# Optimization experiments

Hardware: AMD Instinct MI355X
Metric: run time of the kernel (lower is better)

## Reference

```python
import math
import jax, jax.numpy as jnp
import numpy as np

B, N, D_IN, D_MODEL, H, TOPK = 4, 2048, 256, 512, 8, 32
D_HEAD = D_MODEL // H
EPS = 1e-8


def _linear_params(key, fan_in, fan_out):
    lim = 1.0 / math.sqrt(fan_in)
    kw, kb = jax.random.split(key)
    W = jax.random.uniform(kw, (fan_in, fan_out), minval=-lim, maxval=lim, dtype=jnp.float32)
    b = jax.random.uniform(kb, (fan_out,), minval=-lim, maxval=lim, dtype=jnp.float32)
    return W, b


def setup_inputs() -> dict:
    key = jax.random.key(0)
    kx, ks, kq, kk, kv, ko = jax.random.split(key, 6)
    x = jax.random.normal(kx, (B, N, D_IN), dtype=jnp.float32)
    sim = jax.random.uniform(ks, (B, N, N), dtype=jnp.float32)  # non-negative similarity
    Wq, bq = _linear_params(kq, D_IN, D_MODEL)
    Wk, bk = _linear_params(kk, D_IN, D_MODEL)
    Wv, bv = _linear_params(kv, D_IN, D_MODEL)
    Wo, bo = _linear_params(ko, D_MODEL, D_MODEL)
    tau_raw = jnp.asarray(0.0, dtype=jnp.float32)
    return {"x": x, "sim": sim, "Wq": Wq, "bq": bq, "Wk": Wk, "bk": bk,
            "Wv": Wv, "bv": bv, "Wo": Wo, "bo": bo, "tau_raw": tau_raw}


def reference(x, sim, Wq, bq, Wk, bk, Wv, bv, Wo, bo, tau_raw):
    b, n, _ = x.shape
    # projections -> (B, H, N, d_head)
    def split_heads(t):
        return t.reshape(b, n, H, D_HEAD).transpose(0, 2, 1, 3)
    Qh = split_heads(x @ Wq + bq)
    Kh = split_heads(x @ Wk + bk)
    Vh = split_heads(x @ Wv + bv)

    # top-k masked, row-normalized similarity bias
    simc = jnp.maximum(sim, 0.0)
    diag = jnp.eye(n, dtype=bool)
    sim_for_topk = jnp.where(diag, -jnp.inf, simc)  # exclude self from top-k
    k = min(TOPK, n - 1)
    _, topk_idx = jax.lax.top_k(sim_for_topk, k)  # (B, N, k)
    bidx = jnp.arange(b)[:, None, None]
    ridx = jnp.arange(n)[None, :, None]
    keep = jnp.zeros((b, n, n), dtype=bool).at[bidx, ridx, topk_idx].set(True)
    keep = keep & ~diag
    sim_masked = jnp.where(keep, simc, 0.0)
    rowsum = jnp.maximum(sim_masked.sum(axis=-1, keepdims=True), EPS)
    sim_bias = sim_masked / rowsum  # (B, N, N), rows sum to 1 over kept entries

    tau = jax.nn.softplus(tau_raw)
    scale = 1.0 / math.sqrt(D_HEAD)
    logits = jnp.einsum('bhnd,bhmd->bhnm', Qh, Kh) * scale + tau * sim_bias[:, None, :, :]
    attn = jax.nn.softmax(logits, axis=-1)
    out = jnp.einsum('bhnm,bhmd->bhnd', attn, Vh)
    out = out.transpose(0, 2, 1, 3).reshape(b, n, D_MODEL)
    return out @ Wo + bo
```

## Files before the change

kernel.cpp:

```cpp
#include <hip/hip_runtime.h>

typedef unsigned int u32;
typedef unsigned short u16;
typedef unsigned long long u64;
typedef float f32x4 __attribute__((ext_vector_type(4)));
typedef u32 u32x4 __attribute__((ext_vector_type(4)));
typedef u32 u32x2 __attribute__((ext_vector_type(2)));

#define DEVINL static __device__ __forceinline__
#define LOG2E 1.44269504088896340736f
#define QSCALE 0.18033688011112042f

DEVINL u16 f2bf(float f) {
  u32 u = __builtin_bit_cast(u32, f);
  u32 r = u + 0x7FFFu + ((u >> 16) & 1u);
  return (u16)(r >> 16);
}

DEVINL u32 cvtpk(float lo, float hi) {
  u32 r;
  asm("v_cvt_pk_bf16_f32 %0, %1, %2" : "=v"(r) : "v"(lo), "v"(hi));
  return r;
}
DEVINL float exp2v(float x) {
  float r;
  asm("v_exp_f32 %0, %1" : "=v"(r) : "v"(x));
  return r;
}
DEVINL void mfma_b16(f32x4& c, u32x4 a, u32x4 b) {
  asm volatile("v_mfma_f32_16x16x32_bf16 %0, %1, %2, %0" : "+v"(c) : "v"(a), "v"(b));
}
DEVINL void mfma_fence() { asm volatile("s_nop 7\n\ts_nop 7"); }

DEVINL int mbcnt64(u64 m) {
  return __builtin_amdgcn_mbcnt_hi((u32)(m >> 32), __builtin_amdgcn_mbcnt_lo((u32)m, 0));
}
DEVINL u64 shfl_xor64(u64 v, int m) {
  u32 lo = (u32)v, hi = (u32)(v >> 32);
  lo = __shfl_xor(lo, m, 64);
  hi = __shfl_xor(hi, m, 64);
  return ((u64)hi << 32) | lo;
}

__global__ __launch_bounds__(256) void prep_kernel(
    const float* __restrict__ x, const float* __restrict__ Wq, const float* __restrict__ Wk,
    const float* __restrict__ Wv, const float* __restrict__ Wo, const float* __restrict__ bq,
    const float* __restrict__ bk, const float* __restrict__ bv, u16* __restrict__ xb,
    u16* __restrict__ WqkvT, u16* __restrict__ WoT, float* __restrict__ biasQKV) {
  __shared__ float T[64][65];
  const int blk = blockIdx.x, tid = threadIdx.x;
  if (blk < 1024) {
    int i0 = (blk * 256 + tid) * 8;
    f32x4 v0 = *(const f32x4*)(x + i0);
    f32x4 v1 = *(const f32x4*)(x + i0 + 4);
    u32x4 pk;
    pk[0] = (u32)f2bf(v0[0]) | ((u32)f2bf(v0[1]) << 16);
    pk[1] = (u32)f2bf(v0[2]) | ((u32)f2bf(v0[3]) << 16);
    pk[2] = (u32)f2bf(v1[0]) | ((u32)f2bf(v1[1]) << 16);
    pk[3] = (u32)f2bf(v1[2]) | ((u32)f2bf(v1[3]) << 16);
    *(u32x4*)(xb + i0) = pk;
    return;
  }
  if (blk < 1024 + 96 + 64) {
    int t = blk - 1024;
    const float* W;
    u16* dst;
    int k0, n0, outld, outrow0;
    if (t < 96) {
      int sel = t >> 5, tt = t & 31;
      W = sel == 0 ? Wq : (sel == 1 ? Wk : Wv);
      k0 = (tt >> 3) * 64;
      n0 = (tt & 7) * 64;
      dst = WqkvT;
      outld = 256;
      outrow0 = sel * 512 + n0;
    } else {
      int tt = t - 96;
      W = Wo;
      k0 = (tt >> 3) * 64;
      n0 = (tt & 7) * 64;
      dst = WoT;
      outld = 512;
      outrow0 = n0;
    }
    const int r = tid >> 2, q = tid & 3;
#pragma unroll
    for (int i = 0; i < 4; i++) {
      f32x4 vv = *(const f32x4*)(W + (size_t)(k0 + r) * 512 + n0 + q * 16 + i * 4);
      T[r][q * 16 + i * 4 + 0] = vv[0];
      T[r][q * 16 + i * 4 + 1] = vv[1];
      T[r][q * 16 + i * 4 + 2] = vv[2];
      T[r][q * 16 + i * 4 + 3] = vv[3];
    }
    __syncthreads();
    u16 tmpv[16];
#pragma unroll
    for (int e = 0; e < 16; e++) tmpv[e] = f2bf(T[q * 16 + e][r]);
    u32x4 w0, w1;
#pragma unroll
    for (int j = 0; j < 4; j++) {
      w0[j] = (u32)tmpv[2 * j] | ((u32)tmpv[2 * j + 1] << 16);
      w1[j] = (u32)tmpv[8 + 2 * j] | ((u32)tmpv[9 + 2 * j] << 16);
    }
    u16* dp = dst + (size_t)(outrow0 + r) * outld + k0 + q * 16;
    *(u32x4*)dp = w0;
    *(u32x4*)(dp + 8) = w1;
    return;
  }
  for (int i = tid; i < 1536; i += 256)
    biasQKV[i] = i < 512 ? bq[i] : (i < 1024 ? bk[i - 512] : bv[i - 1024]);
}

__global__ __launch_bounds__(256) void topk_kernel(const float* __restrict__ sim,
                                                   const float* __restrict__ tau_raw,
                                                   u32* __restrict__ tpw,
                                                   u32* __restrict__ tstarts) {
  __shared__ u32 keyA[4][64];
  __shared__ u32 idxA[4][64];
  const int tid = threadIdx.x, lane = tid & 63, w = tid >> 6;
  const int row = blockIdx.x * 4 + w;
  const int b = row >> 11, n = row & 2047;
  const float* src = sim + ((size_t)b * 2048 + n) * 2048;

  u32 keys[32];
#pragma unroll
  for (int q = 0; q < 8; q++) {
    f32x4 v = *(const f32x4*)(src + q * 256 + lane * 4);
#pragma unroll
    for (int j = 0; j < 4; j++) {
      int m = (q << 8) + lane * 4 + j;
      float xv = fmaxf(v[j], 0.f);
      keys[q * 4 + j] = (m == n) ? 0u : (__builtin_bit_cast(u32, xv) + 1u);
    }
  }

  u32 Plo = 1u;
  u32 Phi = 0x7F000000u;
  u32 P = 0x3F7C0001u;
  int c = 0;
  for (int it = 0; it < 40; ++it) {
    int lc = 0;
#pragma unroll
    for (int e = 0; e < 32; e++) lc += (keys[e] >= P) ? 1 : 0;
#pragma unroll
    for (int off = 1; off < 64; off <<= 1) lc += __shfl_xor(lc, off, 64);
    c = lc;
    if (c >= 32 && c <= 64) break;
    if (c < 32) Phi = P; else Plo = P;
    if (Phi - Plo <= 1) break;
    long long Pn;
    if (P >= 0x3F000000u && P <= 0x3F800000u) {
      Pn = (long long)P + (long long)(c - 48) * 4098;
    } else {
      Pn = (long long)Plo + (long long)((Phi - Plo) >> 1);
    }
    if (Pn <= (long long)Plo || Pn >= (long long)Phi)
      Pn = (long long)Plo + (long long)((Phi - Plo) >> 1);
    P = (u32)Pn;
  }

  u32* kws = keyA[w];
  u32* iws = idxA[w];
  int base = 0;
#pragma unroll
  for (int e = 0; e < 32; e++) {
    bool pred = keys[e] >= P;
    u64 mk = __ballot(pred);
    if (pred) {
      int slot = base + mbcnt64(mk);
      if (slot < 64) {
        kws[slot] = keys[e];
        iws[slot] = (u32)((e >> 2) * 256 + lane * 4 + (e & 3));
      }
    }
    base += __popcll(mk);
  }
  for (int s = base + lane; s < 64; s += 64) {
    kws[s] = 0u;
    iws[s] = 2047u;
  }

  u64 K = ((u64)kws[lane] << 11) | (u64)(2047u - iws[lane]);
#pragma unroll
  for (int k = 2; k <= 64; k <<= 1) {
#pragma unroll
    for (int j = k >> 1; j >= 1; j >>= 1) {
      u64 o = shfl_xor64(K, j);
      bool keepmax = (((lane & k) == 0) == ((lane & j) == 0));
      u64 mx = K > o ? K : o;
      u64 mn = K > o ? o : K;
      K = keepmax ? mx : mn;
    }
  }

  u32 key = (u32)(K >> 11);
  int myidx = 2047 - (int)(K & 0x7FFu);
  float myval = __builtin_bit_cast(float, key - 1u);
  float sv = (lane < 32) ? myval : 0.f;
#pragma unroll
  for (int off = 1; off < 64; off <<= 1) sv += __shfl_xor(sv, off, 64);
  float tau = log1pf(__expf(tau_raw[0]));
  float wvv = tau * myval / fmaxf(sv, 1e-8f) * LOG2E;

  int bucket = (myidx >> 2) & 3;
  u64 bm0 = __ballot(lane < 32 && bucket == 0);
  u64 bm1 = __ballot(lane < 32 && bucket == 1);
  u64 bm2 = __ballot(lane < 32 && bucket == 2);
  int c0 = __popcll(bm0), c1 = __popcll(bm1), c2 = __popcll(bm2);
  int key2 = (bucket << 11) | myidx;
  int rank = 0;
  for (int j2 = 0; j2 < 32; j2++) {
    int ok = __shfl(key2, j2, 64);
    rank += (ok < key2) ? 1 : 0;
  }
  if (lane < 32) tpw[(size_t)row * 32 + rank] = ((u32)myidx << 16) | (u32)f2bf(wvv);
  if (lane == 0)
    tstarts[row] = ((u32)c0 << 8) | ((u32)(c0 + c1) << 16) | ((u32)(c0 + c1 + c2) << 24);
}

template <int MODE>
__global__ __launch_bounds__(256) void gemm_nt(const u16* __restrict__ A,
                                               const u16* __restrict__ Bt,
                                               const float* __restrict__ bias,
                                               u16* __restrict__ outQ, u16* __restrict__ outK,
                                               u16* __restrict__ outV, float* __restrict__ outF,
                                               int M, int N, int K) {
  __shared__ __align__(16) u16 As[128 * 32];
  __shared__ __align__(16) u16 Bs[128 * 32];

  const int tid = threadIdx.x;
  const int lane = tid & 63;
  const int w = tid >> 6;
  const int g = lane >> 4, c = lane & 15;
  const int wr = (w >> 1) * 64, wc = (w & 1) * 64;
  const int m0 = blockIdx.y * 128, n0 = blockIdx.x * 128;

  f32x4 acc[4][4];
#pragma unroll
  for (int i = 0; i < 4; i++)
#pragma unroll
    for (int j = 0; j < 4; j++) acc[i][j] = f32x4{0.f, 0.f, 0.f, 0.f};

  const int srow = tid >> 1;
  const int shalf = tid & 1;
  const u16* Arow = A + (size_t)(m0 + srow) * K + shalf * 16;
  const u16* Brow = Bt + (size_t)(n0 + srow) * K + shalf * 16;
  char* asbase = (char*)As;
  char* bsbase = (char*)Bs;
  const u32 swz = (u32)((srow & 7) << 4);
  const u32 wb0 = (u32)(srow * 64 + shalf * 32);

  for (int kt = 0; kt < K; kt += 32) {
    __syncthreads();
    {
      u32x4 a0 = *(const u32x4*)(Arow + kt);
      u32x4 a1 = *(const u32x4*)(Arow + kt + 8);
      u32x4 b0 = *(const u32x4*)(Brow + kt);
      u32x4 b1 = *(const u32x4*)(Brow + kt + 8);
      *(u32x4*)(asbase + ((wb0 + 0) ^ swz)) = a0;
      *(u32x4*)(asbase + ((wb0 + 16) ^ swz)) = a1;
      *(u32x4*)(bsbase + ((wb0 + 0) ^ swz)) = b0;
      *(u32x4*)(bsbase + ((wb0 + 16) ^ swz)) = b1;
    }
    __syncthreads();
    u32x4 af[4], bfr[4];
#pragma unroll
    for (int fr = 0; fr < 4; fr++) {
      int row = wr + fr * 16 + c;
      af[fr] = *(const u32x4*)(asbase + ((u32)(row * 64 + g * 16) ^ ((u32)((row & 7) << 4))));
    }
#pragma unroll
    for (int fc = 0; fc < 4; fc++) {
      int row = wc + fc * 16 + c;
      bfr[fc] = *(const u32x4*)(bsbase + ((u32)(row * 64 + g * 16) ^ ((u32)((row & 7) << 4))));
    }
#pragma unroll
    for (int fr = 0; fr < 4; fr++)
#pragma unroll
      for (int fc = 0; fc < 4; fc++) mfma_b16(acc[fr][fc], af[fr], bfr[fc]);
  }
  mfma_fence();
#pragma unroll
  for (int fc = 0; fc < 4; fc++) {
    int gcol = n0 + wc + fc * 16 + c;
    float bvv = bias[gcol];
#pragma unroll
    for (int fr = 0; fr < 4; fr++) {
#pragma unroll
      for (int r = 0; r < 4; r++) {
        int grow = m0 + wr + fr * 16 + 4 * g + r;
        float v = acc[fr][fc][r] + bvv;
        if (MODE == 0) {
          int sel = gcol >> 9, c9 = gcol & 511;
          if (sel == 0) v *= QSCALE;
          int hh = c9 >> 6, dd = c9 & 63;
          int bb = grow >> 11, nn = grow & 2047;
          size_t off2 = ((size_t)(bb * 8 + hh) * 2048 + nn) * 64 + dd;
          u16* dst = sel == 0 ? outQ : (sel == 1 ? outK : outV);
          dst[off2] = f2bf(v);
        } else {
          outF[(size_t)grow * N + gcol] = v;
        }
      }
    }
  }
}

__global__ __launch_bounds__(256) void transpose_v(const u16* __restrict__ Vb,
                                                   u16* __restrict__ Vt) {
  __shared__ __align__(16) u16 T[64 * 72];
  const int nt = blockIdx.x, bh = blockIdx.y;
  const int tid = threadIdx.x;
  const int rr = tid >> 2, q = tid & 3;
  {
    const u16* src = Vb + ((size_t)bh * 2048 + nt * 64 + rr) * 64 + q * 16;
    u32x4 a = *(const u32x4*)src;
    u32x4 b = *(const u32x4*)(src + 8);
    *(u32x4*)(&T[rr * 72 + q * 16]) = a;
    *(u32x4*)(&T[rr * 72 + q * 16 + 8]) = b;
  }
  __syncthreads();
  {
    union { u16 s[16]; u32x4 v[2]; } ou;
#pragma unroll
    for (int e = 0; e < 16; e++) ou.s[e] = T[(q * 16 + e) * 72 + rr];
    u16* dst = Vt + ((size_t)bh * 64 + rr) * 2048 + nt * 64 + q * 16;
    *(u32x4*)dst = ou.v[0];
    *(u32x4*)(dst + 8) = ou.v[1];
  }
}

__global__ __launch_bounds__(256) void attn_kernel(const u16* __restrict__ Qb,
                                                   const u16* __restrict__ Kb,
                                                   const u16* __restrict__ Vt,
                                                   const u32* __restrict__ tpw,
                                                   const u32* __restrict__ tstarts,
                                                   u16* __restrict__ attnout) {
  __shared__ __align__(16) u16 Ks[64 * 64];
  __shared__ __align__(16) u16 Vs[64 * 64];
  __shared__ __align__(16) u16 Ps[4][16 * 64];

  const int bid = blockIdx.x;
  const int bh = (bid & 7) * 4 + ((bid >> 3) & 3);
  const int qt = bid >> 5;
  const int b = bh >> 3, h = bh & 7;
  const int tid = threadIdx.x, lane = tid & 63, w = tid >> 6;
  const int g = lane >> 4, c = lane & 15;
  const int qbase = qt * 64;
  const int rowl = w * 16 + c;

  const u16* qptr = Qb + ((size_t)bh * 2048 + qbase + rowl) * 64 + g * 8;
  u32x4 aq0 = *(const u32x4*)qptr;
  u32x4 aq1 = *(const u32x4*)(qptr + 32);

  const u32* tpwrow = tpw + ((size_t)b * 2048 + qbase + rowl) * 32;
  u32 stw = tstarts[b * 2048 + qbase + rowl];
  int p = (int)((stw >> (8 * g)) & 255u);
  const int pend = (g == 3) ? 32 : (int)((stw >> (8 * g + 8)) & 255u);
  u32 nextE = (p < pend) ? tpwrow[p] : 0xFFFF0000u;

  float m = -1e30f, ssum = 0.f;
  f32x4 o[4];
#pragma unroll
  for (int db = 0; db < 4; db++) o[db] = f32x4{0.f, 0.f, 0.f, 0.f};

  const int sr = tid >> 2, sq = tid & 3;
  const u16* ksrc = Kb + ((size_t)bh * 2048 + sr) * 64 + sq * 16;
  const u16* vsrc = Vt + ((size_t)bh * 64 + sr) * 2048 + sq * 16;
  char* ksb = (char*)Ks;
  char* vsb = (char*)Vs;
  char* pwb = (char*)&Ps[w][0];
  const u32 sswz = (u32)((sr & 7) << 4);
  const u32 sb0 = (u32)(sr * 128 + sq * 32);

  u32 koff[4][2], poff2[2], pwoff[4];
#pragma unroll
  for (int cb = 0; cb < 4; cb++) {
    int row = cb * 16 + c;
    u32 sz = (u32)((row & 7) << 4);
    koff[cb][0] = ((u32)(row * 128 + g * 16)) ^ sz;
    koff[cb][1] = ((u32)(row * 128 + g * 16 + 64)) ^ sz;
  }
  {
    u32 sz = (u32)((c & 7) << 4);
#pragma unroll
    for (int mm = 0; mm < 2; mm++) poff2[mm] = ((u32)(c * 128 + mm * 64 + g * 16)) ^ sz;
#pragma unroll
    for (int cb = 0; cb < 4; cb++) pwoff[cb] = ((u32)(c * 128 + cb * 32 + g * 8)) ^ sz;
  }

  u32x4 rk0 = *(const u32x4*)ksrc;
  u32x4 rk1 = *(const u32x4*)(ksrc + 8);
  u32x4 rv0 = *(const u32x4*)vsrc;
  u32x4 rv1 = *(const u32x4*)(vsrc + 8);

  for (int t = 0; t < 32; ++t) {
    const int jt = t * 64;
    __syncthreads();
    *(u32x4*)(ksb + ((sb0 + 0) ^ sswz)) = rk0;
    *(u32x4*)(ksb + ((sb0 + 16) ^ sswz)) = rk1;
    *(u32x4*)(vsb + ((sb0 + 0) ^ sswz)) = rv0;
    *(u32x4*)(vsb + ((sb0 + 16) ^ sswz)) = rv1;
    __syncthreads();

    {
      int jt2 = t < 31 ? jt + 64 : 1984;
      const u16* kp = ksrc + (size_t)jt2 * 64;
      const u16* vp = vsrc + jt2;
      rk0 = *(const u32x4*)kp;
      rk1 = *(const u32x4*)(kp + 8);
      rv0 = *(const u32x4*)vp;
      rv1 = *(const u32x4*)(vp + 8);
    }

    __builtin_amdgcn_s_setprio(1);
    f32x4 s[4];
#pragma unroll
    for (int cb = 0; cb < 4; cb++) {
      u32x4 bk0 = *(const u32x4*)(ksb + koff[cb][0]);
      u32x4 bk1 = *(const u32x4*)(ksb + koff[cb][1]);
      f32x4 tacc = f32x4{0.f, 0.f, 0.f, 0.f};
      mfma_b16(tacc, bk0, aq0);
      mfma_b16(tacc, bk1, aq1);
      s[cb] = tacc;
    }
    __builtin_amdgcn_s_setprio(0);
    mfma_fence();

    const int jtend = jt + 64;
    while ((int)(nextE >> 16) < jtend) {
      float wv = __builtin_bit_cast(float, nextE << 16);
      int rel = (int)(nextE >> 16) - jt - 4 * g;
#pragma unroll
      for (int cb = 0; cb < 4; cb++)
#pragma unroll
        for (int r = 0; r < 4; r++) s[cb][r] += (rel == cb * 16 + r) ? wv : 0.f;
      p++;
      nextE = (p < pend) ? tpwrow[p] : 0xFFFF0000u;
    }

    float tm = fmaxf(fmaxf(fmaxf(s[0][0], s[0][1]), fmaxf(s[0][2], s[0][3])),
                     fmaxf(fmaxf(s[1][0], s[1][1]), fmaxf(s[1][2], s[1][3])));
    tm = fmaxf(tm, fmaxf(fmaxf(fmaxf(s[2][0], s[2][1]), fmaxf(s[2][2], s[2][3])),
                         fmaxf(fmaxf(s[3][0], s[3][1]), fmaxf(s[3][2], s[3][3]))));
    tm = fmaxf(tm, __shfl_xor(tm, 16, 64));
    tm = fmaxf(tm, __shfl_xor(tm, 32, 64));
    if (!__all(tm - m <= 8.f)) {
      float mn = fmaxf(m, tm);
      float f = exp2v(m - mn);
      m = mn;
      ssum *= f;
#pragma unroll
      for (int db = 0; db < 4; db++) o[db] *= f;
    }
    float lsum = 0.f;
#pragma unroll
    for (int cb = 0; cb < 4; cb++) {
      float e0 = exp2v(s[cb][0] - m);
      float e1 = exp2v(s[cb][1] - m);
      float e2 = exp2v(s[cb][2] - m);
      float e3 = exp2v(s[cb][3] - m);
      lsum += (e0 + e1) + (e2 + e3);
      u32x2 pk;
      pk[0] = cvtpk(e0, e1);
      pk[1] = cvtpk(e2, e3);
      *(u32x2*)(pwb + pwoff[cb]) = pk;
    }
    ssum += lsum;

    u32x4 pf0 = *(const u32x4*)(pwb + poff2[0]);
    u32x4 pf1 = *(const u32x4*)(pwb + poff2[1]);
    __builtin_amdgcn_s_setprio(1);
#pragma unroll
    for (int db = 0; db < 4; db++) {
      u32x4 bv0 = *(const u32x4*)(vsb + koff[db][0]);
      u32x4 bv1 = *(const u32x4*)(vsb + koff[db][1]);
      mfma_b16(o[db], bv0, pf0);
      mfma_b16(o[db], bv1, pf1);
    }
    __builtin_amdgcn_s_setprio(0);
  }
  mfma_fence();

  ssum += __shfl_xor(ssum, 16, 64);
  ssum += __shfl_xor(ssum, 32, 64);
  float inv = 1.f / ssum;
  const int n = qbase + rowl;
  u16* obase = attnout + ((size_t)b * 2048 + n) * 512 + h * 64 + 4 * g;
#pragma unroll
  for (int db = 0; db < 4; db++) {
    u32x2 st;
    st[0] = cvtpk(o[db][0] * inv, o[db][1] * inv);
    st[1] = cvtpk(o[db][2] * inv, o[db][3] * inv);
    *(u32x2*)(obase + db * 16) = st;
  }
}

extern "C" void kernel_launch(void* const* d_in, const int* in_sizes, int n_in,
                              void* d_out, int out_size, void* d_ws, size_t ws_size,
                              hipStream_t stream) {
  (void)in_sizes; (void)n_in; (void)out_size; (void)ws_size;
  const float* x = (const float*)d_in[0];
  const float* sim = (const float*)d_in[1];
  const float* Wq = (const float*)d_in[2];
  const float* bq = (const float*)d_in[3];
  const float* Wk = (const float*)d_in[4];
  const float* bk = (const float*)d_in[5];
  const float* Wv = (const float*)d_in[6];
  const float* bv = (const float*)d_in[7];
  const float* Wo = (const float*)d_in[8];
  const float* bo = (const float*)d_in[9];
  const float* tau = (const float*)d_in[10];
  float* out = (float*)d_out;

  char* ws = (char*)d_ws;
  size_t off = 0;
  auto alloc = [&](size_t bytes) {
    void* p = ws + off;
    off += (bytes + 255) & ~(size_t)255;
    return p;
  };
  u16* xb = (u16*)alloc((size_t)8192 * 256 * 2);
  u16* WqkvT = (u16*)alloc((size_t)1536 * 256 * 2);
  u16* WoT = (u16*)alloc((size_t)512 * 512 * 2);
  float* biasQKV = (float*)alloc((size_t)1536 * 4);
  u16* Qb = (u16*)alloc((size_t)32 * 2048 * 64 * 2);
  u16* Kb = (u16*)alloc((size_t)32 * 2048 * 64 * 2);
  u16* Vb = (u16*)alloc((size_t)32 * 2048 * 64 * 2);
  u16* Vt = (u16*)alloc((size_t)32 * 2048 * 64 * 2);
  u16* attnout = (u16*)alloc((size_t)8192 * 512 * 2);
  u32* tpw = (u32*)alloc((size_t)8192 * 32 * 4);
  u32* tstarts = (u32*)alloc((size_t)8192 * 4);

  prep_kernel<<<dim3(1185), dim3(256), 0, stream>>>(x, Wq, Wk, Wv, Wo, bq, bk, bv, xb, WqkvT,
                                                    WoT, biasQKV);
  topk_kernel<<<dim3(2048), dim3(256), 0, stream>>>(sim, tau, tpw, tstarts);
  gemm_nt<0><<<dim3(12, 64), dim3(256), 0, stream>>>(xb, WqkvT, biasQKV, Qb, Kb, Vb, nullptr,
                                                     8192, 1536, 256);
  transpose_v<<<dim3(32, 32), dim3(256), 0, stream>>>(Vb, Vt);
  attn_kernel<<<dim3(1024), dim3(256), 0, stream>>>(Qb, Kb, Vt, tpw, tstarts, attnout);
  gemm_nt<1><<<dim3(4, 64), dim3(256), 0, stream>>>(attnout, WoT, bo, nullptr, nullptr, nullptr,
                                                    out, 8192, 512, 512);
}
```

Measured before the change: 250.5 us.

## Split attention key range in two halves and merge partial softmax results

The attention kernel now splits the 2048 keys into two halves, each handled by a separate block, doubling the grid to 2048 blocks. Each block writes unnormalized fp32 partial outputs plus its running max and sum. A new merge kernel combines the two halves with log-sum-exp rescaling. The top-k kernel also emits per-bucket counts of low-half indices so each split starts at the right sparse bias entry. This trades extra global traffic (fp32 partials, about 33MB written and read) and an extra launch for more parallelism and shorter per-block loops.

```diff
diff --git a/kernel.cpp b/kernel.cpp
--- a/kernel.cpp
+++ b/kernel.cpp
@@ -4,6 +4,7 @@
 typedef unsigned short u16;
 typedef unsigned long long u64;
 typedef float f32x4 __attribute__((ext_vector_type(4)));
+typedef float f32x2 __attribute__((ext_vector_type(2)));
 typedef u32 u32x4 __attribute__((ext_vector_type(4)));
 typedef u32 u32x2 __attribute__((ext_vector_type(2)));
 
@@ -114,7 +115,8 @@
 __global__ __launch_bounds__(256) void topk_kernel(const float* __restrict__ sim,
                                                    const float* __restrict__ tau_raw,
                                                    u32* __restrict__ tpw,
-                                                   u32* __restrict__ tstarts) {
+                                                   u32* __restrict__ tstarts,
+                                                   u32* __restrict__ tlo) {
   __shared__ u32 keyA[4][64];
   __shared__ u32 idxA[4][64];
   const int tid = threadIdx.x, lane = tid & 63, w = tid >> 6;
@@ -207,6 +209,11 @@
   u64 bm1 = __ballot(lane < 32 && bucket == 1);
   u64 bm2 = __ballot(lane < 32 && bucket == 2);
   int c0 = __popcll(bm0), c1 = __popcll(bm1), c2 = __popcll(bm2);
+  bool lo = myidx < 1024;
+  u64 l0 = __ballot(lane < 32 && bucket == 0 && lo);
+  u64 l1 = __ballot(lane < 32 && bucket == 1 && lo);
+  u64 l2 = __ballot(lane < 32 && bucket == 2 && lo);
+  u64 l3 = __ballot(lane < 32 && bucket == 3 && lo);
   int key2 = (bucket << 11) | myidx;
   int rank = 0;
   for (int j2 = 0; j2 < 32; j2++) {
@@ -214,8 +221,11 @@
     rank += (ok < key2) ? 1 : 0;
   }
   if (lane < 32) tpw[(size_t)row * 32 + rank] = ((u32)myidx << 16) | (u32)f2bf(wvv);
-  if (lane == 0)
+  if (lane == 0) {
     tstarts[row] = ((u32)c0 << 8) | ((u32)(c0 + c1) << 16) | ((u32)(c0 + c1 + c2) << 24);
+    tlo[row] = (u32)__popcll(l0) | ((u32)__popcll(l1) << 8) | ((u32)__popcll(l2) << 16) |
+               ((u32)__popcll(l3) << 24);
+  }
 }
 
 template <int MODE>
@@ -335,15 +345,19 @@
                                                    const u16* __restrict__ Vt,
                                                    const u32* __restrict__ tpw,
                                                    const u32* __restrict__ tstarts,
-                                                   u16* __restrict__ attnout) {
+                                                   const u32* __restrict__ tlo,
+                                                   float* __restrict__ opart,
+                                                   float* __restrict__ mspart) {
   __shared__ __align__(16) u16 Ks[64 * 64];
   __shared__ __align__(16) u16 Vs[64 * 64];
   __shared__ __align__(16) u16 Ps[4][16 * 64];
 
   const int bid = blockIdx.x;
   const int bh = (bid & 7) * 4 + ((bid >> 3) & 3);
-  const int qt = bid >> 5;
-  const int b = bh >> 3, h = bh & 7;
+  const int split = (bid >> 5) & 1;
+  const int qt = bid >> 6;
+  const int b = bh >> 3;
+  const int kv0 = split * 1024;
   const int tid = threadIdx.x, lane = tid & 63, w = tid >> 6;
   const int g = lane >> 4, c = lane & 15;
   const int qbase = qt * 64;
@@ -353,10 +367,12 @@
   u32x4 aq0 = *(const u32x4*)qptr;
   u32x4 aq1 = *(const u32x4*)(qptr + 32);
 
-  const u32* tpwrow = tpw + ((size_t)b * 2048 + qbase + rowl) * 32;
-  u32 stw = tstarts[b * 2048 + qbase + rowl];
+  const size_t rowgi = (size_t)b * 2048 + qbase + rowl;
+  const u32* tpwrow = tpw + rowgi * 32;
+  u32 stw = tstarts[rowgi];
   int p = (int)((stw >> (8 * g)) & 255u);
   const int pend = (g == 3) ? 32 : (int)((stw >> (8 * g + 8)) & 255u);
+  if (split) p += (int)((tlo[rowgi] >> (8 * g)) & 255u);
   u32 nextE = (p < pend) ? tpwrow[p] : 0xFFFF0000u;
 
   float m = -1e30f, ssum = 0.f;
@@ -365,8 +381,8 @@
   for (int db = 0; db < 4; db++) o[db] = f32x4{0.f, 0.f, 0.f, 0.f};
 
   const int sr = tid >> 2, sq = tid & 3;
-  const u16* ksrc = Kb + ((size_t)bh * 2048 + sr) * 64 + sq * 16;
-  const u16* vsrc = Vt + ((size_t)bh * 64 + sr) * 2048 + sq * 16;
+  const u16* ksrc = Kb + ((size_t)bh * 2048 + kv0 + sr) * 64 + sq * 16;
+  const u16* vsrc = Vt + ((size_t)bh * 64 + sr) * 2048 + kv0 + sq * 16;
   char* ksb = (char*)Ks;
   char* vsb = (char*)Vs;
   char* pwb = (char*)&Ps[w][0];
@@ -394,8 +410,8 @@
   u32x4 rv0 = *(const u32x4*)vsrc;
   u32x4 rv1 = *(const u32x4*)(vsrc + 8);
 
-  for (int t = 0; t < 32; ++t) {
-    const int jt = t * 64;
+  for (int t = 0; t < 16; ++t) {
+    const int jt = kv0 + t * 64;
     __syncthreads();
     *(u32x4*)(ksb + ((sb0 + 0) ^ sswz)) = rk0;
     *(u32x4*)(ksb + ((sb0 + 16) ^ sswz)) = rk1;
@@ -404,9 +420,9 @@
     __syncthreads();
 
     {
-      int jt2 = t < 31 ? jt + 64 : 1984;
-      const u16* kp = ksrc + (size_t)jt2 * 64;
-      const u16* vp = vsrc + jt2;
+      int rel2 = t < 15 ? (t + 1) * 64 : 960;
+      const u16* kp = ksrc + (size_t)rel2 * 64;
+      const u16* vp = vsrc + rel2;
       rk0 = *(const u32x4*)kp;
       rk1 = *(const u32x4*)(kp + 8);
       rv0 = *(const u32x4*)vp;
@@ -484,16 +500,42 @@
 
   ssum += __shfl_xor(ssum, 16, 64);
   ssum += __shfl_xor(ssum, 32, 64);
-  float inv = 1.f / ssum;
-  const int n = qbase + rowl;
-  u16* obase = attnout + ((size_t)b * 2048 + n) * 512 + h * 64 + 4 * g;
-#pragma unroll
-  for (int db = 0; db < 4; db++) {
-    u32x2 st;
-    st[0] = cvtpk(o[db][0] * inv, o[db][1] * inv);
-    st[1] = cvtpk(o[db][2] * inv, o[db][3] * inv);
-    *(u32x2*)(obase + db * 16) = st;
-  }
+  const size_t pbase = ((size_t)split * 32 + bh) * 2048 + qbase + rowl;
+  float* ob = opart + pbase * 64 + 4 * g;
+#pragma unroll
+  for (int db = 0; db < 4; db++) *(f32x4*)(ob + db * 16) = o[db];
+  if (g == 0) {
+    f32x2 msv;
+    msv[0] = m;
+    msv[1] = ssum;
+    *(f32x2*)(mspart + pbase * 2) = msv;
+  }
+}
+
+__global__ __launch_bounds__(256) void merge_kernel(const float* __restrict__ opart,
+                                                    const float* __restrict__ mspart,
+                                                    u16* __restrict__ attnout) {
+  const int idx = blockIdx.x * 256 + threadIdx.x;
+  const int row = idx >> 7;
+  const int c4 = (idx & 127) * 4;
+  const int b = row >> 11, n = row & 2047;
+  const int h = c4 >> 6, d = c4 & 63;
+  const size_t base0 = ((size_t)(b * 8 + h)) * 2048 + n;
+  const size_t base1 = base0 + 32 * 2048;
+  f32x4 o0 = *(const f32x4*)(opart + base0 * 64 + d);
+  f32x4 o1 = *(const f32x4*)(opart + base1 * 64 + d);
+  f32x2 ms0 = *(const f32x2*)(mspart + base0 * 2);
+  f32x2 ms1 = *(const f32x2*)(mspart + base1 * 2);
+  float M = fmaxf(ms0[0], ms1[0]);
+  float sc0 = exp2v(ms0[0] - M);
+  float sc1 = exp2v(ms1[0] - M);
+  float inv = 1.f / (ms0[1] * sc0 + ms1[1] * sc1);
+  sc0 *= inv;
+  sc1 *= inv;
+  u32x2 st;
+  st[0] = cvtpk(o0[0] * sc0 + o1[0] * sc1, o0[1] * sc0 + o1[1] * sc1);
+  st[1] = cvtpk(o0[2] * sc0 + o1[2] * sc1, o0[3] * sc0 + o1[3] * sc1);
+  *(u32x2*)(attnout + (size_t)row * 512 + c4) = st;
 }
 
 extern "C" void kernel_launch(void* const* d_in, const int* in_sizes, int n_in,
@@ -531,14 +573,19 @@
   u16* attnout = (u16*)alloc((size_t)8192 * 512 * 2);
   u32* tpw = (u32*)alloc((size_t)8192 * 32 * 4);
   u32* tstarts = (u32*)alloc((size_t)8192 * 4);
+  u32* tlo = (u32*)alloc((size_t)8192 * 4);
+  float* opart = (float*)alloc((size_t)2 * 32 * 2048 * 64 * 4);
+  float* mspart = (float*)alloc((size_t)2 * 32 * 2048 * 2 * 4);
 
   prep_kernel<<<dim3(1185), dim3(256), 0, stream>>>(x, Wq, Wk, Wv, Wo, bq, bk, bv, xb, WqkvT,
                                                     WoT, biasQKV);
-  topk_kernel<<<dim3(2048), dim3(256), 0, stream>>>(sim, tau, tpw, tstarts);
+  topk_kernel<<<dim3(2048), dim3(256), 0, stream>>>(sim, tau, tpw, tstarts, tlo);
   gemm_nt<0><<<dim3(12, 64), dim3(256), 0, stream>>>(xb, WqkvT, biasQKV, Qb, Kb, Vb, nullptr,
                                                      8192, 1536, 256);
   transpose_v<<<dim3(32, 32), dim3(256), 0, stream>>>(Vb, Vt);
-  attn_kernel<<<dim3(1024), dim3(256), 0, stream>>>(Qb, Kb, Vt, tpw, tstarts, attnout);
+  attn_kernel<<<dim3(2048), dim3(256), 0, stream>>>(Qb, Kb, Vt, tpw, tstarts, tlo, opart,
+                                                    mspart);
+  merge_kernel<<<dim3(4096), dim3(256), 0, stream>>>(opart, mspart, attnout);
   gemm_nt<1><<<dim3(4, 64), dim3(256), 0, stream>>>(attnout, WoT, bo, nullptr, nullptr, nullptr,
                                                     out, 8192, 512, 512);
 }
```

Result: no change. 253.8 us (+1.3%).
